# Performance work log

Measured on AMD Instinct MI355X. Metric: run time of the kernel, lower is better.

Reference implementation:

```python
import jax, jax.numpy as jnp
import numpy as np

S = 2048      # sequence length
E = 2048      # n_embd
H = 16        # n_head
D = E // H    # head_dim = 128
EPS = 1e-5


def _layer_norm(x, w):
    # eqx.nn.LayerNorm, use_bias=False: (x - mean) / sqrt(var + eps) * w
    mu = jnp.mean(x, axis=-1, keepdims=True)
    var = jnp.mean(jnp.square(x - mu), axis=-1, keepdims=True)
    return (x - mu) * jax.lax.rsqrt(var + EPS) * w


def setup_inputs() -> dict:
    key = jax.random.key(0)
    ks = jax.random.split(key, 7)
    x = jax.random.normal(ks[0], (S, E), dtype=jnp.float32)
    # equinox Linear weights are (out_features, in_features); y = W @ x
    w_attn = jax.random.normal(ks[1], (3 * E, E), dtype=jnp.float32) * 0.02
    w_proj_attn = jax.random.normal(ks[2], (E, E), dtype=jnp.float32) * 0.02
    w_fc = jax.random.normal(ks[3], (4 * E, E), dtype=jnp.float32) * 0.02
    w_proj_ffn = jax.random.normal(ks[4], (E, 4 * E), dtype=jnp.float32) * 0.02
    ln1_w = jnp.ones((E,), dtype=jnp.float32)
    ln2_w = jnp.ones((E,), dtype=jnp.float32)
    return {"x": x, "ln1_w": ln1_w, "ln2_w": ln2_w, "w_attn": w_attn,
            "w_proj_attn": w_proj_attn, "w_fc": w_fc, "w_proj_ffn": w_proj_ffn}


def reference(x, ln1_w, ln2_w, w_attn, w_proj_attn, w_fc, w_proj_ffn):
    # --- LN1 + fused QKV projection ---
    h = _layer_norm(x, ln1_w)                       # [S, E]
    qkv = h @ w_attn.T                              # [S, 3E]
    q, k, v = jnp.split(qkv, 3, axis=-1)
    q = q.reshape(S, H, D)
    k = k.reshape(S, H, D)
    v = v.reshape(S, H, D)
    # --- naive causal attention with materialized [H, S, T] scores ---
    scale = 1.0 / jnp.sqrt(jnp.float32(D))
    causal_bias = (jnp.arange(S)[:, None] < jnp.arange(S)[None, :]) * (-10000.0)
    scores = jnp.einsum('shd,thd->hst', q, k) * scale + causal_bias  # [H,S,T]
    probs = jax.nn.softmax(scores, axis=-1)
    attn = jnp.einsum('hst,thd->shd', probs, v).reshape(S, E)
    x = x + attn @ w_proj_attn.T
    # --- LN2 + GELU MLP ---
    h2 = _layer_norm(x, ln2_w)                      # [S, E]
    f = jax.nn.gelu(h2 @ w_fc.T) @ w_proj_ffn.T    # [S,4E] -> [S,E]
    return x + f
```

## Files before the change

### kernel.cpp

```cpp
#include <hip/hip_runtime.h>
#include <hip/hip_bf16.h>

#define S_LEN 2048
#define EMB   2048
#define NH    16
#define HD    128

typedef __bf16 bf16x8 __attribute__((ext_vector_type(8)));
typedef __bf16 bf16x4 __attribute__((ext_vector_type(4)));
typedef float  f32x4  __attribute__((ext_vector_type(4)));
typedef short  s16x4  __attribute__((ext_vector_type(4)));

__device__ __forceinline__ void async_copy16(void* lds, const void* g) {
  __builtin_amdgcn_global_load_lds((__attribute__((address_space(1))) void*)(void*)g,
                                   (__attribute__((address_space(3))) void*)lds, 16, 0, 0);
}

__device__ __forceinline__ unsigned lds_addr(const void* p) {
  return (unsigned)(uintptr_t)(const __attribute__((address_space(3))) char*)p;
}

__device__ __forceinline__ s16x4 tr16(unsigned addr) {
  s16x4 d;
  asm volatile("ds_read_b64_tr_b16 %0, %1" : "=v"(d) : "v"(addr));
  return d;
}

__device__ __forceinline__ float gelu_tanh(float x) {
  float x3 = x * x * x;
  float t  = 0.7978845608028654f * (x + 0.044715f * x3);
  float th = 1.0f - 2.0f / (__expf(2.0f * t) + 1.0f);
  return 0.5f * x * (1.0f + th);
}

__global__ __launch_bounds__(256) void cast_all(const float* __restrict__ s0,
                                                const float* __restrict__ s1,
                                                const float* __restrict__ s2,
                                                const float* __restrict__ s3,
                                                __bf16* __restrict__ d0,
                                                __bf16* __restrict__ d1,
                                                __bf16* __restrict__ d2,
                                                __bf16* __restrict__ d3) {
  size_t i = ((size_t)blockIdx.x * 256 + threadIdx.x) * 4;
  const float* s; __bf16* d; size_t off;
  if (i < 12582912ull)       { s = s0; d = d0; off = i; }
  else if (i < 16777216ull)  { s = s1; d = d1; off = i - 12582912ull; }
  else if (i < 33554432ull)  { s = s2; d = d2; off = i - 16777216ull; }
  else                       { s = s3; d = d3; off = i - 33554432ull; }
  float4 v = *(const float4*)(s + off);
  bf16x4 o;
  o[0] = (__bf16)v.x; o[1] = (__bf16)v.y; o[2] = (__bf16)v.z; o[3] = (__bf16)v.w;
  *(bf16x4*)(d + off) = o;
}

__global__ __launch_bounds__(256) void ln_kernel(const float* __restrict__ x,
                                                 const float* __restrict__ w,
                                                 __bf16* __restrict__ out) {
  int row = blockIdx.x;
  int t = threadIdx.x;
  const float* xr = x + (size_t)row * EMB;
  float4 a = *(const float4*)(xr + t * 8);
  float4 b = *(const float4*)(xr + t * 8 + 4);
  float s  = a.x + a.y + a.z + a.w + b.x + b.y + b.z + b.w;
  float sq = a.x*a.x + a.y*a.y + a.z*a.z + a.w*a.w + b.x*b.x + b.y*b.y + b.z*b.z + b.w*b.w;
  #pragma unroll
  for (int o = 32; o > 0; o >>= 1) { s += __shfl_xor(s, o); sq += __shfl_xor(sq, o); }
  __shared__ float red[8];
  if ((t & 63) == 0) { red[t >> 6] = s; red[(t >> 6) + 4] = sq; }
  __syncthreads();
  s  = red[0] + red[1] + red[2] + red[3];
  sq = red[4] + red[5] + red[6] + red[7];
  float mu  = s * (1.0f / EMB);
  float var = sq * (1.0f / EMB) - mu * mu;
  float rs  = rsqrtf(var + 1e-5f);
  float4 w1 = *(const float4*)(w + t * 8);
  float4 w2 = *(const float4*)(w + t * 8 + 4);
  bf16x8 ov;
  ov[0] = (__bf16)((a.x - mu) * rs * w1.x);
  ov[1] = (__bf16)((a.y - mu) * rs * w1.y);
  ov[2] = (__bf16)((a.z - mu) * rs * w1.z);
  ov[3] = (__bf16)((a.w - mu) * rs * w1.w);
  ov[4] = (__bf16)((b.x - mu) * rs * w2.x);
  ov[5] = (__bf16)((b.y - mu) * rs * w2.y);
  ov[6] = (__bf16)((b.z - mu) * rs * w2.z);
  ov[7] = (__bf16)((b.w - mu) * rs * w2.w);
  *(bf16x8*)(out + (size_t)row * EMB + t * 8) = ov;
}

__global__ __launch_bounds__(256) void ln_fuse_kernel(const float* __restrict__ x,
                                                      const __bf16* __restrict__ part,
                                                      const float* __restrict__ w,
                                                      __bf16* __restrict__ hout,
                                                      float* __restrict__ resout) {
  int row = blockIdx.x;
  int t = threadIdx.x;
  const size_t base = (size_t)row * EMB + t * 8;
  float r[8];
  {
    float4 a = *(const float4*)(x + base);
    float4 b = *(const float4*)(x + base + 4);
    r[0] = a.x; r[1] = a.y; r[2] = a.z; r[3] = a.w;
    r[4] = b.x; r[5] = b.y; r[6] = b.z; r[7] = b.w;
    #pragma unroll
    for (int z = 0; z < 4; z++) {
      bf16x8 p = *(const bf16x8*)(part + (size_t)z * S_LEN * EMB + base);
      #pragma unroll
      for (int k = 0; k < 8; k++) r[k] += (float)p[k];
    }
  }
  float s = 0.f, sq = 0.f;
  #pragma unroll
  for (int k = 0; k < 8; k++) { s += r[k]; sq += r[k] * r[k]; }
  #pragma unroll
  for (int o = 32; o > 0; o >>= 1) { s += __shfl_xor(s, o); sq += __shfl_xor(sq, o); }
  __shared__ float red[8];
  if ((t & 63) == 0) { red[t >> 6] = s; red[(t >> 6) + 4] = sq; }
  __syncthreads();
  s  = red[0] + red[1] + red[2] + red[3];
  sq = red[4] + red[5] + red[6] + red[7];
  float mu  = s * (1.0f / EMB);
  float var = sq * (1.0f / EMB) - mu * mu;
  float rs  = rsqrtf(var + 1e-5f);
  float4 w1 = *(const float4*)(w + t * 8);
  float4 w2 = *(const float4*)(w + t * 8 + 4);
  float wv[8] = {w1.x, w1.y, w1.z, w1.w, w2.x, w2.y, w2.z, w2.w};
  bf16x8 ov;
  #pragma unroll
  for (int k = 0; k < 8; k++) ov[k] = (__bf16)((r[k] - mu) * rs * wv[k]);
  *(bf16x8*)(hout + base) = ov;
  float4 o1 = make_float4(r[0], r[1], r[2], r[3]);
  float4 o2 = make_float4(r[4], r[5], r[6], r[7]);
  *(float4*)(resout + base) = o1;
  *(float4*)(resout + base + 4) = o2;
}

__global__ __launch_bounds__(256) void add4_kernel(float* __restrict__ out,
                                                   const __bf16* __restrict__ part) {
  size_t i = ((size_t)blockIdx.x * 256 + threadIdx.x) * 4;
  float4 o = *(const float4*)(out + i);
  #pragma unroll
  for (int z = 0; z < 4; z++) {
    bf16x4 p = *(const bf16x4*)(part + (size_t)z * S_LEN * EMB + i);
    o.x += (float)p[0]; o.y += (float)p[1]; o.z += (float)p[2]; o.w += (float)p[3];
  }
  *(float4*)(out + i) = o;
}

#define MFMA16(AV, BV, MG)                                                                   \
  _Pragma("unroll")                                                                          \
  for (int m = 0; m < 4; m++)                                                                \
    _Pragma("unroll")                                                                        \
    for (int n = 0; n < 4; n++)                                                              \
      acc[(MG) * 4 + m][n] =                                                                 \
          __builtin_amdgcn_mfma_f32_16x16x32_bf16(AV[m], BV[n], acc[(MG) * 4 + m][n], 0, 0, 0);

#define PHASE_TOP()                                                                          \
  __builtin_amdgcn_s_barrier();                                                              \
  __builtin_amdgcn_s_setprio(1);

#define PHASE_BOT()                                                                          \
  __builtin_amdgcn_s_setprio(0);                                                             \
  __builtin_amdgcn_s_barrier();

template <int EPI>
__global__ __launch_bounds__(512, 2) void gemm256(const __bf16* __restrict__ A,
                                                  const __bf16* __restrict__ B,
                                                  void* __restrict__ Cv,
                                                  int M, int N, int K, int Ksl,
                                                  int NN, int NSPLIT) {
  __shared__ __bf16 As[2 * 2 * 256 * 32];
  __shared__ __bf16 Bs[2 * 2 * 256 * 32];

  const int t = threadIdx.x, w = t >> 6, l = t & 63;
  const int fr = l & 15, g = l >> 4;
  const int wr = w >> 2, wc = w & 3;

  const int nwg = gridDim.x;
  const int wg = (blockIdx.x & 7) * (nwg >> 3) + (blockIdx.x >> 3);
  const int z = wg % NSPLIT;
  const int tile = wg / NSPLIT;
  const int my = tile / NN, nx = tile - my * NN;
  const int m0 = my * 256, n0 = nx * 256;
  const int kb = z * Ksl;
  const int NT = Ksl >> 6;

  const int srow = t >> 2;
  const int schunk = (t & 3) ^ ((t >> 3) & 3);
  const __bf16* Abase = A + (size_t)(m0 + srow) * K + kb + schunk * 8;
  const __bf16* Bbase = B + (size_t)(n0 + srow) * K + kb + schunk * 8;
  const size_t K128 = (size_t)128 * K;
  __bf16* AsT = &As[t * 8];
  __bf16* BsT = &Bs[t * 8];

  auto stage = [&](const __bf16* base, __bf16* dstT, int kt, int kh) {
    const __bf16* src = base + kt * 64 + kh * 32;
    __bf16* dst = dstT + ((kt & 1) * 2 + kh) * 8192;
    async_copy16(dst, src);
    async_copy16(dst + 4096, src + K128);
  };

  const int gran = (g ^ ((fr >> 1) & 3)) << 3;
  auto rdA = [&](bf16x8* dst, int kt, int kh, int mg) {
    const int ub = ((kt & 1) * 2 + kh) * 256;
    #pragma unroll
    for (int m = 0; m < 4; m++) {
      int row = wr * 128 + (mg * 4 + m) * 16 + fr;
      dst[m] = *(const bf16x8*)&As[(ub + row) * 32 + gran];
    }
  };
  auto rdB = [&](bf16x8* dst, int kt, int kh) {
    const int ub = ((kt & 1) * 2 + kh) * 256;
    #pragma unroll
    for (int n = 0; n < 4; n++) {
      int row = wc * 64 + n * 16 + fr;
      dst[n] = *(const bf16x8*)&Bs[(ub + row) * 32 + gran];
    }
  };

  f32x4 acc[8][4] = {};
  bf16x8 av[4], bX[4], bY[4];

  stage(Abase, AsT, 0, 0); stage(Bbase, BsT, 0, 0);
  stage(Abase, AsT, 0, 1); stage(Bbase, BsT, 0, 1);
  if (NT > 1) { stage(Abase, AsT, 1, 0); stage(Bbase, BsT, 1, 0); }
  asm volatile("s_waitcnt vmcnt(4)" ::: "memory");
  __builtin_amdgcn_s_barrier();

  for (int kt = 0; kt < NT; ++kt) {
    const bool s1 = (kt + 1 < NT), s2 = (kt + 2 < NT);
    rdB(bX, kt, 0);
    rdA(av, kt, 0, 0);
    if (s1) stage(Abase, AsT, kt + 1, 1);
    PHASE_TOP();
    MFMA16(av, bX, 0);
    PHASE_BOT();
    rdA(av, kt, 0, 1);
    if (s1) stage(Bbase, BsT, kt + 1, 1);
    PHASE_TOP();
    MFMA16(av, bX, 1);
    __builtin_amdgcn_s_setprio(0);
    if (s1) { asm volatile("s_waitcnt vmcnt(4)" ::: "memory"); }
    else    { asm volatile("s_waitcnt vmcnt(0)" ::: "memory"); }
    __builtin_amdgcn_s_barrier();
    rdB(bY, kt, 1);
    rdA(av, kt, 1, 0);
    if (s2) stage(Abase, AsT, kt + 2, 0);
    PHASE_TOP();
    MFMA16(av, bY, 0);
    PHASE_BOT();
    rdA(av, kt, 1, 1);
    if (s2) stage(Bbase, BsT, kt + 2, 0);
    PHASE_TOP();
    MFMA16(av, bY, 1);
    PHASE_BOT();
  }

  const size_t zoff = (size_t)z * M * N;
  #pragma unroll
  for (int m = 0; m < 8; m++)
    #pragma unroll
    for (int n = 0; n < 4; n++)
      #pragma unroll
      for (int j = 0; j < 4; j++) {
        int orow = m0 + wr * 128 + m * 16 + g * 4 + j;
        int ocol = n0 + wc * 64 + n * 16 + fr;
        size_t idx = (size_t)orow * N + ocol;
        float v = acc[m][n][j];
        if (EPI == 0) {
          ((__bf16*)Cv)[idx] = (__bf16)v;
        } else if (EPI == 2) {
          ((__bf16*)Cv)[idx] = (__bf16)gelu_tanh(v);
        } else {
          ((__bf16*)Cv)[zoff + idx] = (__bf16)v;
        }
      }
}

template <int EPI>
__global__ __launch_bounds__(512, 4) void gemm128(const __bf16* __restrict__ A,
                                                  const __bf16* __restrict__ B,
                                                  void* __restrict__ Cv,
                                                  int M, int N, int K, int Ksl,
                                                  int NN, int NSPLIT) {
  __shared__ __bf16 As[3][128 * 32];
  __shared__ __bf16 Bs[3][256 * 32];

  const int t = threadIdx.x, w = t >> 6, l = t & 63;
  const int fr = l & 15, g = l >> 4;
  const int wr = w >> 2, wc = w & 3;

  const int nwg = gridDim.x;
  const int wg = (blockIdx.x & 7) * (nwg >> 3) + (blockIdx.x >> 3);
  const int z = wg % NSPLIT;
  const int tile = wg / NSPLIT;
  const int my = tile / NN, nx = tile - my * NN;
  const int m0 = my * 128, n0 = nx * 256;
  const int kb = z * Ksl;
  const int NT = Ksl >> 5;

  const int srow = t >> 2;
  const int schunk = (t & 3) ^ ((t >> 3) & 3);
  const __bf16* Abase = A + (size_t)(m0 + srow) * K + kb + schunk * 8;
  const __bf16* Bbase = B + (size_t)(n0 + srow) * K + kb + schunk * 8;
  const size_t K128 = (size_t)128 * K;

  auto stage = [&](int kt, int slot) {
    const __bf16* sa = Abase + kt * 32;
    const __bf16* sb = Bbase + kt * 32;
    async_copy16(&As[slot][t * 8], sa);
    async_copy16(&Bs[slot][t * 8], sb);
    async_copy16(&Bs[slot][t * 8 + 4096], sb + K128);
  };

  const int gran = (g ^ ((fr >> 1) & 3)) << 3;

  f32x4 acc[4][4] = {};

  stage(0, 0);
  stage(1, 1);
  asm volatile("s_waitcnt vmcnt(3)" ::: "memory");
  __builtin_amdgcn_s_barrier();

  int sc = 0, s1 = 1, s2 = 2;
  for (int kt = 0; kt < NT; ++kt) {
    bf16x8 a[4], b[4];
    #pragma unroll
    for (int m = 0; m < 4; m++)
      a[m] = *(const bf16x8*)&As[sc][(wr * 64 + m * 16 + fr) * 32 + gran];
    #pragma unroll
    for (int n = 0; n < 4; n++)
      b[n] = *(const bf16x8*)&Bs[sc][(wc * 64 + n * 16 + fr) * 32 + gran];
    if (kt + 2 < NT) stage(kt + 2, s2);
    __builtin_amdgcn_s_setprio(1);
    #pragma unroll
    for (int m = 0; m < 4; m++)
      #pragma unroll
      for (int n = 0; n < 4; n++)
        acc[m][n] = __builtin_amdgcn_mfma_f32_16x16x32_bf16(a[m], b[n], acc[m][n], 0, 0, 0);
    __builtin_amdgcn_s_setprio(0);
    if (kt + 1 < NT) {
      if (kt + 2 < NT) { asm volatile("s_waitcnt vmcnt(3)" ::: "memory"); }
      else             { asm volatile("s_waitcnt vmcnt(0)" ::: "memory"); }
    }
    __builtin_amdgcn_s_barrier();
    int tmp = sc; sc = s1; s1 = s2; s2 = tmp;
  }

  const size_t zoff = (size_t)z * M * N;
  #pragma unroll
  for (int m = 0; m < 4; m++)
    #pragma unroll
    for (int n = 0; n < 4; n++)
      #pragma unroll
      for (int j = 0; j < 4; j++) {
        int orow = m0 + wr * 64 + m * 16 + g * 4 + j;
        int ocol = n0 + wc * 64 + n * 16 + fr;
        size_t idx = (size_t)orow * N + ocol;
        float v = acc[m][n][j];
        if (EPI == 0) {
          ((__bf16*)Cv)[idx] = (__bf16)v;
        } else if (EPI == 2) {
          ((__bf16*)Cv)[idx] = (__bf16)gelu_tanh(v);
        } else {
          ((__bf16*)Cv)[zoff + idx] = (__bf16)v;
        }
      }
}

__global__ __launch_bounds__(512, 2) void attn_kernel(const __bf16* __restrict__ qkv,
                                                      __bf16* __restrict__ out) {
  __shared__ __bf16 Kt[2][64 * 128];
  __shared__ __bf16 Vt[2][64 * 128];
  __shared__ __bf16 Pb[8][16 * 64];

  const int bid = blockIdx.x;
  const int h = bid & 15;
  const int pi = bid >> 4;
  const int qbA = pi, qbB = 31 - pi;

  const int t = threadIdx.x, w = t >> 6, l = t & 63;
  const int g = l >> 4, fr = l & 15;
  const int fkb = g * 8;
  const int myqb = (w < 4) ? qbA : qbB;
  const int q0 = myqb * 64 + (w & 3) * 16;
  const float scale = 0.08838834764831845f;

  const int kchunk = fr ^ ((w * 4 + g) & 7);
  const int vkey = (l >> 1) & 3;
  const int vd0  = (l >> 3) * 16 + (l & 1) * 8;

  const size_t row3E = (size_t)(3 * EMB);
  const __bf16* Kg = qkv + EMB + h * HD;
  const __bf16* Vg = qkv + 2 * EMB + h * HD;

  bf16x8 qf[4];
  #pragma unroll
  for (int kc = 0; kc < 4; kc++)
    qf[kc] = *(const bf16x8*)&qkv[(size_t)(q0 + fr) * row3E + h * HD + kc * 32 + fkb];

  f32x4 o[8] = {};
  float mrun[4] = {-1e30f, -1e30f, -1e30f, -1e30f};
  float lsum[4] = {0.f, 0.f, 0.f, 0.f};

  const unsigned vtrb[2] = { lds_addr(&Vt[0][0]) + g * 2048 + fr * 8,
                             lds_addr(&Vt[1][0]) + g * 2048 + fr * 8 };

  auto stage = [&](int buf, int it) {
    const int t0 = it * 64;
    #pragma unroll
    for (int r = 0; r < 2; r++) {
      async_copy16(&Kt[buf][(r * 8 + w) * 512],
                   Kg + (size_t)(t0 + (r * 8 + w) * 4 + g) * row3E + kchunk * 8);
      async_copy16(&Vt[buf][(r * 8 + w) * 512],
                   Vg + (size_t)(t0 + (r * 8 + w) * 4 + vkey) * row3E + vd0);
    }
  };

  const int nt = qbB + 1;
  stage(0, 0);
  int cur = 0;

  for (int it = 0; it < nt; it++) {
    __syncthreads();
    if (it + 1 < nt) stage(cur ^ 1, it + 1);

    if (it <= myqb) {
      const int t0 = it * 64;
      f32x4 s[4] = {};
      __builtin_amdgcn_s_setprio(1);
      #pragma unroll
      for (int n = 0; n < 4; n++)
        #pragma unroll
        for (int kc = 0; kc < 4; kc++) {
          bf16x8 kf = *(const bf16x8*)&Kt[cur][(n * 16 + fr) * 128 +
                                              (((kc * 4 + g) ^ (fr & 7)) << 3)];
          s[n] = __builtin_amdgcn_mfma_f32_16x16x32_bf16(qf[kc], kf, s[n], 0, 0, 0);
        }
      __builtin_amdgcn_s_setprio(0);
      #pragma unroll
      for (int n = 0; n < 4; n++)
        #pragma unroll
        for (int j = 0; j < 4; j++) {
          int tcol = t0 + n * 16 + fr;
          int qrow = q0 + g * 4 + j;
          float v = s[n][j] * scale;
          s[n][j] = (tcol > qrow) ? -1e30f : v;
        }
      float pm[4];
      #pragma unroll
      for (int j = 0; j < 4; j++) {
        pm[j] = fmaxf(fmaxf(s[0][j], s[1][j]), fmaxf(s[2][j], s[3][j]));
        #pragma unroll
        for (int off = 1; off < 16; off <<= 1) pm[j] = fmaxf(pm[j], __shfl_xor(pm[j], off));
      }
      float factor[4];
      #pragma unroll
      for (int j = 0; j < 4; j++) {
        float mn = fmaxf(mrun[j], pm[j]);
        factor[j] = __expf(mrun[j] - mn);
        mrun[j] = mn;
      }
      float rs[4] = {0.f, 0.f, 0.f, 0.f};
      #pragma unroll
      for (int n = 0; n < 4; n++)
        #pragma unroll
        for (int j = 0; j < 4; j++) {
          float p = __expf(s[n][j] - mrun[j]);
          s[n][j] = p;
          rs[j] += p;
        }
      #pragma unroll
      for (int j = 0; j < 4; j++) {
        #pragma unroll
        for (int off = 1; off < 16; off <<= 1) rs[j] += __shfl_xor(rs[j], off);
        lsum[j] = lsum[j] * factor[j] + rs[j];
      }
      #pragma unroll
      for (int b = 0; b < 8; b++)
        #pragma unroll
        for (int j = 0; j < 4; j++) o[b][j] *= factor[j];

      #pragma unroll
      for (int n = 0; n < 4; n++)
        #pragma unroll
        for (int j = 0; j < 4; j++) {
          int q   = g * 4 + j;
          int key = n * 16 + fr;
          int cs  = (key >> 3) ^ (q & 7);
          Pb[w][q * 64 + cs * 8 + (key & 7)] = (__bf16)s[n][j];
        }

      bf16x8 pf[2];
      #pragma unroll
      for (int kc = 0; kc < 2; kc++)
        pf[kc] = *(const bf16x8*)&Pb[w][fr * 64 + (((kc * 4 + g) ^ (fr & 7)) << 3)];

      const unsigned vtr = vtrb[cur];
      __builtin_amdgcn_s_setprio(1);
      #pragma unroll
      for (int b = 0; b < 8; b++) {
        s16x4 t00 = tr16(vtr + b * 128);
        s16x4 t01 = tr16(vtr + b * 128 + 1024);
        s16x4 t10 = tr16(vtr + b * 128 + 8192);
        s16x4 t11 = tr16(vtr + b * 128 + 8192 + 1024);
        asm volatile("s_waitcnt lgkmcnt(0)");
        __builtin_amdgcn_sched_barrier(0);
        union { s16x4 hh[2]; bf16x8 v; } u0, u1;
        u0.hh[0] = t00; u0.hh[1] = t01;
        u1.hh[0] = t10; u1.hh[1] = t11;
        o[b] = __builtin_amdgcn_mfma_f32_16x16x32_bf16(pf[0], u0.v, o[b], 0, 0, 0);
        o[b] = __builtin_amdgcn_mfma_f32_16x16x32_bf16(pf[1], u1.v, o[b], 0, 0, 0);
      }
      __builtin_amdgcn_s_setprio(0);
    }
    cur ^= 1;
  }

  float rcp[4];
  #pragma unroll
  for (int j = 0; j < 4; j++) rcp[j] = 1.0f / lsum[j];
  #pragma unroll
  for (int b = 0; b < 8; b++)
    #pragma unroll
    for (int j = 0; j < 4; j++) {
      int qrow = q0 + g * 4 + j;
      out[(size_t)qrow * EMB + h * HD + b * 16 + fr] = (__bf16)(o[b][j] * rcp[j]);
    }
}

extern "C" void kernel_launch(void* const* d_in, const int* in_sizes, int n_in,
                              void* d_out, int out_size, void* d_ws, size_t ws_size,
                              hipStream_t stream) {
  const float* x     = (const float*)d_in[0];
  const float* ln1w  = (const float*)d_in[1];
  const float* ln2w  = (const float*)d_in[2];
  const float* wattn = (const float*)d_in[3];
  const float* wproja= (const float*)d_in[4];
  const float* wfc   = (const float*)d_in[5];
  const float* wprojf= (const float*)d_in[6];
  float* out = (float*)d_out;
  char* ws = (char*)d_ws;

  __bf16* wattn_b  = (__bf16*)(ws);
  __bf16* wproja_b = (__bf16*)(ws + 25165824);
  __bf16* wfc_b    = (__bf16*)(ws + 33554432);
  __bf16* wprojf_b = (__bf16*)(ws + 67108864);
  __bf16* h_b      = (__bf16*)(ws + 100663296);
  __bf16* qkv_b    = (__bf16*)(ws + 109051904);
  __bf16* attn_b   = (__bf16*)(ws + 134217728);
  __bf16* f1_b     = (__bf16*)(ws + 142606336);
  __bf16* p1_part  = f1_b;
  __bf16* p2_part  = qkv_b;

  cast_all<<<49152, 256, 0, stream>>>(wattn, wproja, wfc, wprojf,
                                      wattn_b, wproja_b, wfc_b, wprojf_b);

  ln_kernel<<<S_LEN, 256, 0, stream>>>(x, ln1w, h_b);
  gemm256<0><<<192, 512, 0, stream>>>(h_b, wattn_b, qkv_b, S_LEN, 3 * EMB, EMB, EMB, 24, 1);
  attn_kernel<<<dim3(256), 512, 0, stream>>>(qkv_b, attn_b);
  gemm256<5><<<256, 512, 0, stream>>>(attn_b, wproja_b, p1_part, S_LEN, EMB, EMB, EMB / 4, 8, 4);
  ln_fuse_kernel<<<S_LEN, 256, 0, stream>>>(x, p1_part, ln2w, h_b, out);
  gemm128<2><<<512, 512, 0, stream>>>(h_b, wfc_b, f1_b, S_LEN, 4 * EMB, EMB, EMB, 32, 1);
  gemm128<5><<<512, 512, 0, stream>>>(f1_b, wprojf_b, p2_part, S_LEN, EMB, 4 * EMB, 2048, 8, 4);
  add4_kernel<<<4096, 256, 0, stream>>>(out, p2_part);
}
```

Before: 413.7 us.

## Merge weight cast with LN1 and swap GEMM tile sizes across projections

Merges the fp32-to-bf16 weight cast kernel and the first LayerNorm kernel into one prologue launch, with extra blocks handling the LN rows. It also switches the attention-output projection to the 128-tile GEMM and the two MLP GEMMs to the 256-tile GEMM, changing grid sizes and per-block work. The intent is to cut one launch and give each GEMM a tile size better matched to its shape, at the risk of worse occupancy or load balance for some GEMMs.

```diff
diff --git a/kernel.cpp b/kernel.cpp
--- a/kernel.cpp
+++ b/kernel.cpp
@@ -33,31 +33,32 @@
   return 0.5f * x * (1.0f + th);
 }
 
-__global__ __launch_bounds__(256) void cast_all(const float* __restrict__ s0,
-                                                const float* __restrict__ s1,
-                                                const float* __restrict__ s2,
-                                                const float* __restrict__ s3,
-                                                __bf16* __restrict__ d0,
-                                                __bf16* __restrict__ d1,
-                                                __bf16* __restrict__ d2,
-                                                __bf16* __restrict__ d3) {
-  size_t i = ((size_t)blockIdx.x * 256 + threadIdx.x) * 4;
-  const float* s; __bf16* d; size_t off;
-  if (i < 12582912ull)       { s = s0; d = d0; off = i; }
-  else if (i < 16777216ull)  { s = s1; d = d1; off = i - 12582912ull; }
-  else if (i < 33554432ull)  { s = s2; d = d2; off = i - 16777216ull; }
-  else                       { s = s3; d = d3; off = i - 33554432ull; }
-  float4 v = *(const float4*)(s + off);
-  bf16x4 o;
-  o[0] = (__bf16)v.x; o[1] = (__bf16)v.y; o[2] = (__bf16)v.z; o[3] = (__bf16)v.w;
-  *(bf16x4*)(d + off) = o;
-}
-
-__global__ __launch_bounds__(256) void ln_kernel(const float* __restrict__ x,
-                                                 const float* __restrict__ w,
-                                                 __bf16* __restrict__ out) {
-  int row = blockIdx.x;
-  int t = threadIdx.x;
+__global__ __launch_bounds__(256) void prologue_kernel(const float* __restrict__ s0,
+                                                       const float* __restrict__ s1,
+                                                       const float* __restrict__ s2,
+                                                       const float* __restrict__ s3,
+                                                       __bf16* __restrict__ d0,
+                                                       __bf16* __restrict__ d1,
+                                                       __bf16* __restrict__ d2,
+                                                       __bf16* __restrict__ d3,
+                                                       const float* __restrict__ x,
+                                                       const float* __restrict__ lnw,
+                                                       __bf16* __restrict__ lnout) {
+  const int t = threadIdx.x;
+  if (blockIdx.x < 49152) {
+    size_t i = ((size_t)blockIdx.x * 256 + t) * 4;
+    const float* s; __bf16* d; size_t off;
+    if (i < 12582912ull)       { s = s0; d = d0; off = i; }
+    else if (i < 16777216ull)  { s = s1; d = d1; off = i - 12582912ull; }
+    else if (i < 33554432ull)  { s = s2; d = d2; off = i - 16777216ull; }
+    else                       { s = s3; d = d3; off = i - 33554432ull; }
+    float4 v = *(const float4*)(s + off);
+    bf16x4 o;
+    o[0] = (__bf16)v.x; o[1] = (__bf16)v.y; o[2] = (__bf16)v.z; o[3] = (__bf16)v.w;
+    *(bf16x4*)(d + off) = o;
+    return;
+  }
+  int row = blockIdx.x - 49152;
   const float* xr = x + (size_t)row * EMB;
   float4 a = *(const float4*)(xr + t * 8);
   float4 b = *(const float4*)(xr + t * 8 + 4);
@@ -73,8 +74,8 @@
   float mu  = s * (1.0f / EMB);
   float var = sq * (1.0f / EMB) - mu * mu;
   float rs  = rsqrtf(var + 1e-5f);
-  float4 w1 = *(const float4*)(w + t * 8);
-  float4 w2 = *(const float4*)(w + t * 8 + 4);
+  float4 w1 = *(const float4*)(lnw + t * 8);
+  float4 w2 = *(const float4*)(lnw + t * 8 + 4);
   bf16x8 ov;
   ov[0] = (__bf16)((a.x - mu) * rs * w1.x);
   ov[1] = (__bf16)((a.y - mu) * rs * w1.y);
@@ -84,7 +85,7 @@
   ov[5] = (__bf16)((b.y - mu) * rs * w2.y);
   ov[6] = (__bf16)((b.z - mu) * rs * w2.z);
   ov[7] = (__bf16)((b.w - mu) * rs * w2.w);
-  *(bf16x8*)(out + (size_t)row * EMB + t * 8) = ov;
+  *(bf16x8*)(lnout + (size_t)row * EMB + t * 8) = ov;
 }
 
 __global__ __launch_bounds__(256) void ln_fuse_kernel(const float* __restrict__ x,
@@ -552,15 +553,14 @@
   __bf16* p1_part  = f1_b;
   __bf16* p2_part  = qkv_b;
 
-  cast_all<<<49152, 256, 0, stream>>>(wattn, wproja, wfc, wprojf,
-                                      wattn_b, wproja_b, wfc_b, wprojf_b);
-
-  ln_kernel<<<S_LEN, 256, 0, stream>>>(x, ln1w, h_b);
+  prologue_kernel<<<51200, 256, 0, stream>>>(wattn, wproja, wfc, wprojf,
+                                             wattn_b, wproja_b, wfc_b, wprojf_b,
+                                             x, ln1w, h_b);
   gemm256<0><<<192, 512, 0, stream>>>(h_b, wattn_b, qkv_b, S_LEN, 3 * EMB, EMB, EMB, 24, 1);
   attn_kernel<<<dim3(256), 512, 0, stream>>>(qkv_b, attn_b);
-  gemm256<5><<<256, 512, 0, stream>>>(attn_b, wproja_b, p1_part, S_LEN, EMB, EMB, EMB / 4, 8, 4);
+  gemm128<5><<<512, 512, 0, stream>>>(attn_b, wproja_b, p1_part, S_LEN, EMB, EMB, EMB / 4, 8, 4);
   ln_fuse_kernel<<<S_LEN, 256, 0, stream>>>(x, p1_part, ln2w, h_b, out);
-  gemm128<2><<<512, 512, 0, stream>>>(h_b, wfc_b, f1_b, S_LEN, 4 * EMB, EMB, EMB, 32, 1);
-  gemm128<5><<<512, 512, 0, stream>>>(f1_b, wprojf_b, p2_part, S_LEN, EMB, 4 * EMB, 2048, 8, 4);
+  gemm256<2><<<256, 512, 0, stream>>>(h_b, wfc_b, f1_b, S_LEN, 4 * EMB, EMB, EMB, 32, 1);
+  gemm256<5><<<256, 512, 0, stream>>>(f1_b, wprojf_b, p2_part, S_LEN, EMB, 4 * EMB, 2048, 8, 4);
   add4_kernel<<<4096, 256, 0, stream>>>(out, p2_part);
 }
```

Measured after the change: 395.3 us, median of 2. 1.05x faster.
